# Kernel optimization log

Hardware: AMD Instinct MI355X
Metric: run time of the kernel (lower is better)

The kernel has to match this reference:

```python
import jax, jax.numpy as jnp
import numpy as np

N_NODES = 40000
N_EDGES = 320000
N_GRAPHS = 64
IN_DIM = 128
HID4 = 256   # hidden_dim * 4
OUT_DIM = 128
LN_EPS = 1e-5


def setup_inputs() -> dict:
    key = jax.random.key(0)
    ks = jax.random.split(key, 12)
    x = jax.random.normal(ks[0], (N_NODES, IN_DIM), dtype=jnp.float32)
    w = jax.random.uniform(ks[1], (N_EDGES, 4), dtype=jnp.float32)
    src = jax.random.randint(ks[2], (N_EDGES,), 0, N_NODES, dtype=jnp.int32)
    dst = jax.random.randint(ks[3], (N_EDGES,), 0, N_NODES, dtype=jnp.int32)
    graph_ids = jnp.sort(jax.random.randint(ks[4], (N_NODES,), 0, N_GRAPHS, dtype=jnp.int32))
    # parameters (no biases on GraphConv / fc1 linear)
    W1 = jax.random.normal(ks[5], (IN_DIM, HID4), dtype=jnp.float32) / np.sqrt(IN_DIM)
    fc1_W = jax.random.normal(ks[6], (IN_DIM, HID4), dtype=jnp.float32) / np.sqrt(IN_DIM)
    ln_gamma = jnp.ones((HID4,), dtype=jnp.float32)
    ln_beta = jnp.zeros((HID4,), dtype=jnp.float32)
    W2 = jax.random.normal(ks[7], (2 * HID4, HID4), dtype=jnp.float32) / np.sqrt(2 * HID4)
    W3 = jax.random.normal(ks[8], (HID4, OUT_DIM), dtype=jnp.float32) / np.sqrt(HID4)
    return {"x": x, "w": w, "W1": W1, "fc1_W": fc1_W, "ln_gamma": ln_gamma,
            "ln_beta": ln_beta, "W2": W2, "W3": W3,
            "src": src, "dst": dst, "graph_ids": graph_ids}


def _graph_conv(feat, src, dst, ew, W, out_inv_sqrt, in_inv_sqrt):
    # DGL GraphConv, norm='both', bias=False, with scalar edge_weight:
    # h = D_out^{-1/2} x ; m_e = w_e * h[src] ; agg = scatter_add(m, dst) ;
    # out = (D_in^{-1/2} agg) @ W
    h = feat * out_inv_sqrt[:, None]
    m = h[src] * ew[:, None]                       # [E, D] messages
    agg = jax.ops.segment_sum(m, dst, num_segments=N_NODES)
    return (agg * in_inv_sqrt[:, None]) @ W


def reference(x, w, W1, fc1_W, ln_gamma, ln_beta, W2, W3, src, dst, graph_ids):
    # unweighted degree normalization (DGL uses structural degrees, clamp(min=1))
    ones_e = jnp.ones((N_EDGES,), dtype=x.dtype)
    out_deg = jnp.maximum(jax.ops.segment_sum(ones_e, src, num_segments=N_NODES), 1.0)
    in_deg = jnp.maximum(jax.ops.segment_sum(ones_e, dst, num_segments=N_NODES), 1.0)
    out_inv = out_deg ** -0.5
    in_inv = in_deg ** -0.5

    ew = jnp.max(w, axis=1)                        # [E]

    x1 = jax.nn.relu(_graph_conv(x, src, dst, ew, W1, out_inv, in_inv))

    # fc1: Linear(no bias) -> LayerNorm(affine) -> ReLU
    f1 = x @ fc1_W
    mu = jnp.mean(f1, axis=-1, keepdims=True)
    var = jnp.mean((f1 - mu) ** 2, axis=-1, keepdims=True)
    f1 = (f1 - mu) * jax.lax.rsqrt(var + LN_EPS) * ln_gamma + ln_beta
    f1 = jax.nn.relu(f1)

    x1f1 = jnp.concatenate([x1, f1], axis=1)       # [N, 512]
    x2 = jax.nn.relu(_graph_conv(x1f1, src, dst, ew, W2, out_inv, in_inv))
    x3 = jax.nn.relu(_graph_conv(x2, src, dst, ew, W3, out_inv, in_inv))

    # dgl.sum_nodes over batched graph, then row-wise L2 normalize
    readout = jax.ops.segment_sum(x3, graph_ids, num_segments=N_GRAPHS)  # [G, OUT_DIM]
    norm = jnp.maximum(jnp.linalg.norm(readout, axis=1, keepdims=True), 1e-12)
    return readout / norm
```

## Files before the change

### kernel.cpp

```cpp
#include <hip/hip_runtime.h>

#define N_NODES 40000
#define M_PAD   40064
#define N_EDGES 320000
#define N_GRAPHS 64
#define IN_DIM 128
#define HID4 256
#define OUT_DIM 128
#define LN_EPS 1e-5f

typedef short  s16x8  __attribute__((ext_vector_type(8)));
typedef short  s16x4  __attribute__((ext_vector_type(4)));
typedef __bf16 bf16x8 __attribute__((ext_vector_type(8)));
typedef float  f32x4  __attribute__((ext_vector_type(4)));

__device__ __forceinline__ unsigned short f2b(float f) {
    unsigned int u = __builtin_bit_cast(unsigned int, f);
    u += 0x7fffu + ((u >> 16) & 1u);
    return (unsigned short)(u >> 16);
}
__device__ __forceinline__ float b2f(unsigned short h) {
    unsigned int u = (unsigned int)h << 16;
    return __builtin_bit_cast(float, u);
}


__global__ void edge_prep(const float* __restrict__ w, const int* __restrict__ src,
                          const int* __restrict__ dst, float* __restrict__ ew,
                          int* __restrict__ cnt_out, int* __restrict__ cnt_in) {
    int e = blockIdx.x * 256 + threadIdx.x;
    if (e >= N_EDGES) return;
    float4 v = ((const float4*)w)[e];
    ew[e] = fmaxf(fmaxf(v.x, v.y), fmaxf(v.z, v.w));
    atomicAdd(&cnt_out[src[e]], 1);
    atomicAdd(&cnt_in[dst[e]], 1);
}

__global__ void scan_part(const int* __restrict__ cnt, int* __restrict__ partial) {
    int b = blockIdx.x;
    int s = 0;
    for (int i = threadIdx.x; i < 1000; i += 256) s += cnt[b * 1000 + i];
#pragma unroll
    for (int m = 1; m < 64; m <<= 1) s += __shfl_xor(s, m);
    __shared__ int wsm[4];
    if ((threadIdx.x & 63) == 0) wsm[threadIdx.x >> 6] = s;
    __syncthreads();
    if (threadIdx.x == 0) partial[b] = wsm[0] + wsm[1] + wsm[2] + wsm[3];
}

__global__ void scan_final(const int* __restrict__ cnt_in, const int* __restrict__ cnt_out,
                           const int* __restrict__ partial, int* __restrict__ off,
                           float* __restrict__ out_inv, float* __restrict__ in_inv) {
    int b = blockIdx.x, tid = threadIdx.x;
    int lane = tid & 63, wv = tid >> 6;
    int pre = 0;
    for (int j = 0; j < b; ++j) pre += partial[j];
    int i = b * 1000 + tid;
    int v = (tid < 1000) ? cnt_in[i] : 0;
    int x = v;
#pragma unroll
    for (int ofs = 1; ofs < 64; ofs <<= 1) {
        int t = __shfl_up(x, ofs);
        if (lane >= ofs) x += t;
    }
    __shared__ int wsum[16];
    if (lane == 63) wsum[wv] = x;
    __syncthreads();
    if (wv == 0 && lane < 16) {
        int s = wsum[lane];
#pragma unroll
        for (int ofs = 1; ofs < 16; ofs <<= 1) {
            int t = __shfl_up(s, ofs);
            if (lane >= ofs) s += t;
        }
        wsum[lane] = s;
    }
    __syncthreads();
    int incl = pre + (wv > 0 ? wsum[wv - 1] : 0) + x;
    if (tid < 1000) {
        off[i] = incl - v;
        in_inv[i] = rsqrtf(fmaxf((float)v, 1.0f));
        out_inv[i] = rsqrtf(fmaxf((float)cnt_out[i], 1.0f));
    }
    if (b == 39 && tid == 999) off[N_NODES] = incl;
}

__global__ void csr_fill(const int* __restrict__ src, const int* __restrict__ dst,
                         const float* __restrict__ ew, const float* __restrict__ out_inv,
                         const int* __restrict__ off, int* __restrict__ cnt_in,
                         int* __restrict__ srcs, float* __restrict__ ewp,
                         float* __restrict__ ewps) {
    int e = blockIdx.x * 256 + threadIdx.x;
    if (e >= N_EDGES) return;
    int d = dst[e];
    int slot = off[d] + atomicSub(&cnt_in[d], 1) - 1;
    int s = src[e];
    float wv = ew[e];
    srcs[slot] = s;
    ewp[slot] = wv;
    ewps[slot] = wv * out_inv[s];
}


#define XN (N_NODES * IN_DIM)

__global__ void cvt_all(const float* __restrict__ x, const float* __restrict__ W1,
                        const float* __restrict__ fc1, const float* __restrict__ W2,
                        const float* __restrict__ W3, unsigned short* __restrict__ xb,
                        unsigned short* __restrict__ W1t, unsigned short* __restrict__ fc1t,
                        unsigned short* __restrict__ W2t, unsigned short* __restrict__ W3t) {
    int idx = blockIdx.x * 256 + threadIdx.x;
    if (idx < XN) { xb[idx] = f2b(x[idx]); return; }
    int j = idx - XN;
    if (j < 32768) { int k = j >> 8, n = j & 255; W1t[n * 128 + k] = f2b(W1[j]); return; }
    j -= 32768;
    if (j < 32768) { int k = j >> 8, n = j & 255; fc1t[n * 128 + k] = f2b(fc1[j]); return; }
    j -= 32768;
    if (j < 131072) { int k = j >> 8, n = j & 255; W2t[n * 512 + k] = f2b(W2[j]); return; }
    j -= 131072;
    if (j < 32768) { int k = j >> 7, n = j & 127; W3t[n * 256 + k] = f2b(W3[j]); }
}


template <int D, int RELU, int OUT_BF16>
__global__ void gather_nodes(const unsigned short* __restrict__ h, const int* __restrict__ off,
                             const int* __restrict__ srcs, const float* __restrict__ ews,
                             const float* __restrict__ scale, void* __restrict__ outp) {
    int n = blockIdx.x;
    int t = threadIdx.x;
    int b = off[n], e = off[n + 1];
    const unsigned int* hu = (const unsigned int*)h;
    float a0 = 0.0f, a1 = 0.0f;
    int i = b;
    for (; i + 1 < e; i += 2) {
        unsigned int p0 = hu[(size_t)srcs[i] * (D / 2) + t];
        unsigned int p1 = hu[(size_t)srcs[i + 1] * (D / 2) + t];
        float w0 = ews[i], w1 = ews[i + 1];
        a0 += w0 * b2f((unsigned short)p0) + w1 * b2f((unsigned short)p1);
        a1 += w0 * b2f((unsigned short)(p0 >> 16)) + w1 * b2f((unsigned short)(p1 >> 16));
    }
    if (i < e) {
        unsigned int p = hu[(size_t)srcs[i] * (D / 2) + t];
        float w0 = ews[i];
        a0 += w0 * b2f((unsigned short)p);
        a1 += w0 * b2f((unsigned short)(p >> 16));
    }
    float sc = scale[n];
    a0 *= sc; a1 *= sc;
    if (RELU) { a0 = fmaxf(a0, 0.0f); a1 = fmaxf(a1, 0.0f); }
    if (OUT_BF16) {
        unsigned int o = (unsigned int)f2b(a0) | ((unsigned int)f2b(a1) << 16);
        ((unsigned int*)outp)[(size_t)n * (D / 2) + t] = o;
    } else {
        ((float2*)outp)[(size_t)n * (D / 2) + t] = make_float2(a0, a1);
    }
}


template <int RELU, int SCALE_C>
__global__ __launch_bounds__(256) void gemm_mfma(
    const unsigned short* __restrict__ A, const unsigned short* __restrict__ A2,
    const unsigned short* __restrict__ Bt, unsigned short* __restrict__ C,
    const float* __restrict__ rowScaleC, int K1, int K2, int N) {
    __shared__ short As[128][40];
    __shared__ short Bs[128][40];
    const int K = K1 + K2;
    int tid = threadIdx.x;
    int lane = tid & 63, wave = tid >> 6;
    int wm = (wave >> 1) * 64, wn = (wave & 1) * 64;
    int quad = lane >> 4, r16 = lane & 15;
    int m0 = blockIdx.x * 128, n0 = blockIdx.y * 128;

    f32x4 acc[4][4] = {};

    int ra = tid >> 2;
    int ca = (tid & 3) * 8;

    for (int k0 = 0; k0 < K; k0 += 32) {
#pragma unroll
        for (int h = 0; h < 2; ++h) {
            int r = ra + h * 64;
            int kk = k0 + ca;
            const unsigned short* Ap = (kk < K1)
                ? A  + (size_t)(m0 + r) * K1 + kk
                : A2 + (size_t)(m0 + r) * K2 + (kk - K1);
            *(s16x8*)&As[r][ca] = *(const s16x8*)Ap;
            *(s16x8*)&Bs[r][ca] = *(const s16x8*)(Bt + (size_t)(n0 + r) * K + kk);
        }
        __syncthreads();
        s16x8 af[4], bfr[4];
#pragma unroll
        for (int i = 0; i < 4; ++i) af[i]  = *(const s16x8*)&As[wm + i * 16 + r16][quad * 8];
#pragma unroll
        for (int j = 0; j < 4; ++j) bfr[j] = *(const s16x8*)&Bs[wn + j * 16 + r16][quad * 8];
#pragma unroll
        for (int i = 0; i < 4; ++i)
#pragma unroll
            for (int j = 0; j < 4; ++j)
                acc[i][j] = __builtin_amdgcn_mfma_f32_16x16x32_bf16(
                    __builtin_bit_cast(bf16x8, af[i]), __builtin_bit_cast(bf16x8, bfr[j]),
                    acc[i][j], 0, 0, 0);
        __syncthreads();
    }

#pragma unroll
    for (int i = 0; i < 4; ++i) {
        int mbase = m0 + wm + i * 16 + quad * 4;
#pragma unroll
        for (int r = 0; r < 4; ++r) {
            int m = mbase + r;
            float sc = SCALE_C ? rowScaleC[m] : 1.0f;
#pragma unroll
            for (int j = 0; j < 4; ++j) {
                float v = acc[i][j][r] * sc;
                if (RELU) v = fmaxf(v, 0.0f);
                C[(size_t)m * N + n0 + wn + j * 16 + r16] = f2b(v);
            }
        }
    }
}


__global__ void ln_relu_bf16(unsigned short* __restrict__ f, const float* __restrict__ gamma,
                             const float* __restrict__ beta) {
    int row = (blockIdx.x * 256 + threadIdx.x) >> 6;
    int lane = threadIdx.x & 63;
    if (row >= N_NODES) return;
    s16x4* fr = (s16x4*)(f + (size_t)row * HID4);
    s16x4 pv = fr[lane];
    float v0 = b2f((unsigned short)pv[0]);
    float v1 = b2f((unsigned short)pv[1]);
    float v2 = b2f((unsigned short)pv[2]);
    float v3 = b2f((unsigned short)pv[3]);
    float sum = v0 + v1 + v2 + v3;
#pragma unroll
    for (int m = 1; m < 64; m <<= 1) sum += __shfl_xor(sum, m);
    float mu = sum * (1.0f / HID4);
    float d0 = v0 - mu, d1 = v1 - mu, d2 = v2 - mu, d3 = v3 - mu;
    float sq = d0 * d0 + d1 * d1 + d2 * d2 + d3 * d3;
#pragma unroll
    for (int m = 1; m < 64; m <<= 1) sq += __shfl_xor(sq, m);
    float rs = rsqrtf(sq * (1.0f / HID4) + LN_EPS);
    int c = lane * 4;
    s16x4 ov;
    ov[0] = (short)f2b(fmaxf(d0 * rs * gamma[c + 0] + beta[c + 0], 0.0f));
    ov[1] = (short)f2b(fmaxf(d1 * rs * gamma[c + 1] + beta[c + 1], 0.0f));
    ov[2] = (short)f2b(fmaxf(d2 * rs * gamma[c + 2] + beta[c + 2], 0.0f));
    ov[3] = (short)f2b(fmaxf(d3 * rs * gamma[c + 3] + beta[c + 3], 0.0f));
    fr[lane] = ov;
}


#define RO_NPB 16

__global__ void readout_sum(const float* __restrict__ x3, const int* __restrict__ gid,
                            float* __restrict__ ro) {
    int d = threadIdx.x;
    int n0 = blockIdx.x * RO_NPB;
    int n1 = n0 + RO_NPB;
    if (n1 > N_NODES) n1 = N_NODES;
    float acc = 0.0f;
    int cur = gid[n0];
    for (int n = n0; n < n1; ++n) {
        int g = gid[n];
        if (g != cur) {
            atomicAdd(&ro[cur * OUT_DIM + d], acc);
            acc = 0.0f;
            cur = g;
        }
        acc += x3[(size_t)n * OUT_DIM + d];
    }
    atomicAdd(&ro[cur * OUT_DIM + d], acc);
}

__global__ void normalize_out(const float* __restrict__ ro, float* __restrict__ out) {
    int g = blockIdx.x;
    int d = threadIdx.x;
    float v = ro[g * OUT_DIM + d];
    float ss = v * v;
#pragma unroll
    for (int m = 1; m < 64; m <<= 1) ss += __shfl_xor(ss, m);
    __shared__ float s2[2];
    if ((d & 63) == 0) s2[d >> 6] = ss;
    __syncthreads();
    float tot = s2[0] + s2[1];
    float norm = fmaxf(sqrtf(tot), 1e-12f);
    out[g * OUT_DIM + d] = v / norm;
}


extern "C" void kernel_launch(void* const* d_in, const int* in_sizes, int n_in,
                              void* d_out, int out_size, void* d_ws, size_t ws_size,
                              hipStream_t stream) {
    const float* x    = (const float*)d_in[0];
    const float* w    = (const float*)d_in[1];
    const float* W1   = (const float*)d_in[2];
    const float* fc1W = (const float*)d_in[3];
    const float* gam  = (const float*)d_in[4];
    const float* bet  = (const float*)d_in[5];
    const float* W2   = (const float*)d_in[6];
    const float* W3   = (const float*)d_in[7];
    const int* src = (const int*)d_in[8];
    const int* dst = (const int*)d_in[9];
    const int* gid = (const int*)d_in[10];
    float* out = (float*)d_out;

    float* ws = (float*)d_ws;
    float* out_inv = ws + 0;
    float* in_inv  = ws + 40000;
    float* ew      = ws + 80000;
    float* ro      = ws + 400000;
    unsigned short* W1t  = (unsigned short*)(ws + 410000);
    unsigned short* fc1t = (unsigned short*)(ws + 426384);
    unsigned short* W2t  = (unsigned short*)(ws + 442768);
    unsigned short* W3t  = (unsigned short*)(ws + 508304);
    int* cnt_out = (int*)(ws + 524688);
    int* cnt_in  = (int*)(ws + 564688);
    int* partial = (int*)(ws + 604688);
    int* off     = (int*)(ws + 604728);
    int* srcs    = (int*)(ws + 644730);
    float* ewp   = ws + 964730;
    float* ewps  = ws + 1284730;
    unsigned short* xb    = (unsigned short*)(ws + 1650000);
    unsigned short* Q3b   = xb;
    unsigned short* agg1b = (unsigned short*)(ws + 4250000);
    unsigned short* x2b   = agg1b;
    unsigned short* x1b   = (unsigned short*)(ws + 9400000);
    float*          x3    = (float*)x1b;
    unsigned short* f1b   = (unsigned short*)(ws + 14550000);
    unsigned short* P2b   = (unsigned short*)(ws + 19700000);

    hipMemsetAsync(cnt_out, 0, 2 * 40000 * sizeof(int), stream);
    hipMemsetAsync(ro, 0, (size_t)N_GRAPHS * OUT_DIM * sizeof(float), stream);

    cvt_all<<<(XN + 229376 + 255) / 256, 256, 0, stream>>>(x, W1, fc1W, W2, W3,
                                                           xb, W1t, fc1t, W2t, W3t);

    edge_prep<<<(N_EDGES + 255) / 256, 256, 0, stream>>>(w, src, dst, ew, cnt_out, cnt_in);
    scan_part<<<40, 256, 0, stream>>>(cnt_in, partial);
    scan_final<<<40, 1024, 0, stream>>>(cnt_in, cnt_out, partial, off, out_inv, in_inv);
    csr_fill<<<(N_EDGES + 255) / 256, 256, 0, stream>>>(src, dst, ew, out_inv, off, cnt_in,
                                                        srcs, ewp, ewps);

    gather_nodes<IN_DIM, 0, 1><<<N_NODES, IN_DIM / 2, 0, stream>>>(xb, off, srcs, ewps, in_inv, agg1b);
    {
        dim3 grid(M_PAD / 128, HID4 / 128);
        gemm_mfma<1, 0><<<grid, 256, 0, stream>>>(agg1b, nullptr, W1t, x1b, nullptr,
                                                  IN_DIM, 0, HID4);
    }

    {
        dim3 grid(M_PAD / 128, HID4 / 128);
        gemm_mfma<0, 0><<<grid, 256, 0, stream>>>(xb, nullptr, fc1t, f1b, nullptr,
                                                  IN_DIM, 0, HID4);
    }
    ln_relu_bf16<<<N_NODES / 4, 256, 0, stream>>>(f1b, gam, bet);

    {
        dim3 grid(M_PAD / 128, HID4 / 128);
        gemm_mfma<0, 1><<<grid, 256, 0, stream>>>(x1b, f1b, W2t, P2b, out_inv,
                                                  HID4, HID4, HID4);
    }
    gather_nodes<HID4, 1, 1><<<N_NODES, HID4 / 2, 0, stream>>>(P2b, off, srcs, ewp, in_inv, x2b);

    {
        dim3 grid(M_PAD / 128, OUT_DIM / 128);
        gemm_mfma<0, 1><<<grid, 256, 0, stream>>>(x2b, nullptr, W3t, Q3b, out_inv,
                                                  HID4, 0, OUT_DIM);
    }
    gather_nodes<OUT_DIM, 1, 0><<<N_NODES, OUT_DIM / 2, 0, stream>>>(Q3b, off, srcs, ewp, in_inv, x3);

    readout_sum<<<(N_NODES + RO_NPB - 1) / RO_NPB, 128, 0, stream>>>(x3, gid, ro);
    normalize_out<<<N_GRAPHS, 128, 0, stream>>>(ro, out);
}
```

Baseline: 303.8 us.

## Fuse prep kernels, pack edge arrays, merge first GEMMs, unroll gathers

Merges the weight/feature conversion and edge preparation into one kernel, and folds the two memsets into one. CSR edges are stored as packed (src, weight) int2 pairs so each gather reads one 8-byte record instead of two separate arrays. The gather loop is unrolled four-wide for more memory-level parallelism. The two first-layer GEMMs run as one launch using blockIdx.z, and the final layer output is kept in bf16 for readout. This trades some precision in the last layer and extra edge storage for fewer launches and fewer memory transactions.

```diff
diff --git a/kernel.cpp b/kernel.cpp
--- a/kernel.cpp
+++ b/kernel.cpp
@@ -25,15 +25,35 @@
 }
 
 
-__global__ void edge_prep(const float* __restrict__ w, const int* __restrict__ src,
-                          const int* __restrict__ dst, float* __restrict__ ew,
-                          int* __restrict__ cnt_out, int* __restrict__ cnt_in) {
-    int e = blockIdx.x * 256 + threadIdx.x;
-    if (e >= N_EDGES) return;
-    float4 v = ((const float4*)w)[e];
-    ew[e] = fmaxf(fmaxf(v.x, v.y), fmaxf(v.z, v.w));
-    atomicAdd(&cnt_out[src[e]], 1);
-    atomicAdd(&cnt_in[dst[e]], 1);
+#define XN (N_NODES * IN_DIM)
+#define WN 229376
+#define PREP_TOT (XN + WN + N_EDGES)
+
+__global__ void prep_all(const float* __restrict__ x, const float* __restrict__ W1,
+                         const float* __restrict__ fc1, const float* __restrict__ W2,
+                         const float* __restrict__ W3, const float* __restrict__ w,
+                         const int* __restrict__ src, const int* __restrict__ dst,
+                         unsigned short* __restrict__ xb, unsigned short* __restrict__ W1t,
+                         unsigned short* __restrict__ fc1t, unsigned short* __restrict__ W2t,
+                         unsigned short* __restrict__ W3t, float* __restrict__ ew,
+                         int* __restrict__ cnt_out, int* __restrict__ cnt_in) {
+    int idx = blockIdx.x * 256 + threadIdx.x;
+    if (idx < XN) { xb[idx] = f2b(x[idx]); return; }
+    int j = idx - XN;
+    if (j < 32768) { int k = j >> 8, n = j & 255; W1t[n * 128 + k] = f2b(W1[j]); return; }
+    j -= 32768;
+    if (j < 32768) { int k = j >> 8, n = j & 255; fc1t[n * 128 + k] = f2b(fc1[j]); return; }
+    j -= 32768;
+    if (j < 131072) { int k = j >> 8, n = j & 255; W2t[n * 512 + k] = f2b(W2[j]); return; }
+    j -= 131072;
+    if (j < 32768) { int k = j >> 7, n = j & 127; W3t[n * 256 + k] = f2b(W3[j]); return; }
+    j -= 32768;
+    if (j < N_EDGES) {
+        float4 v = ((const float4*)w)[j];
+        ew[j] = fmaxf(fmaxf(v.x, v.y), fmaxf(v.z, v.w));
+        atomicAdd(&cnt_out[src[j]], 1);
+        atomicAdd(&cnt_in[dst[j]], 1);
+    }
 }
 
 __global__ void scan_part(const int* __restrict__ cnt, int* __restrict__ partial) {
@@ -88,72 +108,53 @@
 __global__ void csr_fill(const int* __restrict__ src, const int* __restrict__ dst,
                          const float* __restrict__ ew, const float* __restrict__ out_inv,
                          const int* __restrict__ off, int* __restrict__ cnt_in,
-                         int* __restrict__ srcs, float* __restrict__ ewp,
-                         float* __restrict__ ewps) {
+                         int2* __restrict__ es1, int2* __restrict__ es23) {
     int e = blockIdx.x * 256 + threadIdx.x;
     if (e >= N_EDGES) return;
     int d = dst[e];
     int slot = off[d] + atomicSub(&cnt_in[d], 1) - 1;
     int s = src[e];
     float wv = ew[e];
-    srcs[slot] = s;
-    ewp[slot] = wv;
-    ewps[slot] = wv * out_inv[s];
-}
-
-
-#define XN (N_NODES * IN_DIM)
-
-__global__ void cvt_all(const float* __restrict__ x, const float* __restrict__ W1,
-                        const float* __restrict__ fc1, const float* __restrict__ W2,
-                        const float* __restrict__ W3, unsigned short* __restrict__ xb,
-                        unsigned short* __restrict__ W1t, unsigned short* __restrict__ fc1t,
-                        unsigned short* __restrict__ W2t, unsigned short* __restrict__ W3t) {
-    int idx = blockIdx.x * 256 + threadIdx.x;
-    if (idx < XN) { xb[idx] = f2b(x[idx]); return; }
-    int j = idx - XN;
-    if (j < 32768) { int k = j >> 8, n = j & 255; W1t[n * 128 + k] = f2b(W1[j]); return; }
-    j -= 32768;
-    if (j < 32768) { int k = j >> 8, n = j & 255; fc1t[n * 128 + k] = f2b(fc1[j]); return; }
-    j -= 32768;
-    if (j < 131072) { int k = j >> 8, n = j & 255; W2t[n * 512 + k] = f2b(W2[j]); return; }
-    j -= 131072;
-    if (j < 32768) { int k = j >> 7, n = j & 127; W3t[n * 256 + k] = f2b(W3[j]); }
-}
-
-
-template <int D, int RELU, int OUT_BF16>
+    es1[slot] = make_int2(s, __float_as_int(wv * out_inv[s]));
+    es23[slot] = make_int2(s, __float_as_int(wv));
+}
+
+
+template <int D, int RELU>
 __global__ void gather_nodes(const unsigned short* __restrict__ h, const int* __restrict__ off,
-                             const int* __restrict__ srcs, const float* __restrict__ ews,
-                             const float* __restrict__ scale, void* __restrict__ outp) {
+                             const int2* __restrict__ eg, const float* __restrict__ scale,
+                             unsigned short* __restrict__ outb) {
     int n = blockIdx.x;
     int t = threadIdx.x;
     int b = off[n], e = off[n + 1];
     const unsigned int* hu = (const unsigned int*)h;
     float a0 = 0.0f, a1 = 0.0f;
     int i = b;
-    for (; i + 1 < e; i += 2) {
-        unsigned int p0 = hu[(size_t)srcs[i] * (D / 2) + t];
-        unsigned int p1 = hu[(size_t)srcs[i + 1] * (D / 2) + t];
-        float w0 = ews[i], w1 = ews[i + 1];
-        a0 += w0 * b2f((unsigned short)p0) + w1 * b2f((unsigned short)p1);
-        a1 += w0 * b2f((unsigned short)(p0 >> 16)) + w1 * b2f((unsigned short)(p1 >> 16));
-    }
-    if (i < e) {
-        unsigned int p = hu[(size_t)srcs[i] * (D / 2) + t];
-        float w0 = ews[i];
+    for (; i + 3 < e; i += 4) {
+        int2 e0 = eg[i], e1 = eg[i + 1], e2 = eg[i + 2], e3 = eg[i + 3];
+        unsigned int p0 = hu[(size_t)e0.x * (D / 2) + t];
+        unsigned int p1 = hu[(size_t)e1.x * (D / 2) + t];
+        unsigned int p2 = hu[(size_t)e2.x * (D / 2) + t];
+        unsigned int p3 = hu[(size_t)e3.x * (D / 2) + t];
+        float w0 = __int_as_float(e0.y), w1 = __int_as_float(e1.y);
+        float w2 = __int_as_float(e2.y), w3 = __int_as_float(e3.y);
+        a0 += w0 * b2f((unsigned short)p0) + w1 * b2f((unsigned short)p1)
+            + w2 * b2f((unsigned short)p2) + w3 * b2f((unsigned short)p3);
+        a1 += w0 * b2f((unsigned short)(p0 >> 16)) + w1 * b2f((unsigned short)(p1 >> 16))
+            + w2 * b2f((unsigned short)(p2 >> 16)) + w3 * b2f((unsigned short)(p3 >> 16));
+    }
+    for (; i < e; ++i) {
+        int2 ee = eg[i];
+        unsigned int p = hu[(size_t)ee.x * (D / 2) + t];
+        float w0 = __int_as_float(ee.y);
         a0 += w0 * b2f((unsigned short)p);
         a1 += w0 * b2f((unsigned short)(p >> 16));
     }
     float sc = scale[n];
     a0 *= sc; a1 *= sc;
     if (RELU) { a0 = fmaxf(a0, 0.0f); a1 = fmaxf(a1, 0.0f); }
-    if (OUT_BF16) {
-        unsigned int o = (unsigned int)f2b(a0) | ((unsigned int)f2b(a1) << 16);
-        ((unsigned int*)outp)[(size_t)n * (D / 2) + t] = o;
-    } else {
-        ((float2*)outp)[(size_t)n * (D / 2) + t] = make_float2(a0, a1);
-    }
+    unsigned int o = (unsigned int)f2b(a0) | ((unsigned int)f2b(a1) << 16);
+    ((unsigned int*)outb)[(size_t)n * (D / 2) + t] = o;
 }
 
 
@@ -172,7 +173,6 @@
     int m0 = blockIdx.x * 128, n0 = blockIdx.y * 128;
 
     f32x4 acc[4][4] = {};
-
     int ra = tid >> 2;
     int ca = (tid & 3) * 8;
 
@@ -215,6 +215,68 @@
                 float v = acc[i][j][r] * sc;
                 if (RELU) v = fmaxf(v, 0.0f);
                 C[(size_t)m * N + n0 + wn + j * 16 + r16] = f2b(v);
+            }
+        }
+    }
+}
+
+
+__global__ __launch_bounds__(256) void gemm_dual(
+    const unsigned short* __restrict__ A0, const unsigned short* __restrict__ B0,
+    unsigned short* __restrict__ C0,
+    const unsigned short* __restrict__ A1, const unsigned short* __restrict__ B1,
+    unsigned short* __restrict__ C1) {
+    const unsigned short* A  = blockIdx.z ? A1 : A0;
+    const unsigned short* Bt = blockIdx.z ? B1 : B0;
+    unsigned short* C        = blockIdx.z ? C1 : C0;
+    const int relu = (blockIdx.z == 0);
+    __shared__ short As[128][40];
+    __shared__ short Bs[128][40];
+    int tid = threadIdx.x;
+    int lane = tid & 63, wave = tid >> 6;
+    int wm = (wave >> 1) * 64, wn = (wave & 1) * 64;
+    int quad = lane >> 4, r16 = lane & 15;
+    int m0 = blockIdx.x * 128, n0 = blockIdx.y * 128;
+
+    f32x4 acc[4][4] = {};
+    int ra = tid >> 2;
+    int ca = (tid & 3) * 8;
+
+    for (int k0 = 0; k0 < 128; k0 += 32) {
+#pragma unroll
+        for (int h = 0; h < 2; ++h) {
+            int r = ra + h * 64;
+            int kk = k0 + ca;
+            *(s16x8*)&As[r][ca] = *(const s16x8*)(A + (size_t)(m0 + r) * 128 + kk);
+            *(s16x8*)&Bs[r][ca] = *(const s16x8*)(Bt + (size_t)(n0 + r) * 128 + kk);
+        }
+        __syncthreads();
+        s16x8 af[4], bfr[4];
+#pragma unroll
+        for (int i = 0; i < 4; ++i) af[i]  = *(const s16x8*)&As[wm + i * 16 + r16][quad * 8];
+#pragma unroll
+        for (int j = 0; j < 4; ++j) bfr[j] = *(const s16x8*)&Bs[wn + j * 16 + r16][quad * 8];
+#pragma unroll
+        for (int i = 0; i < 4; ++i)
+#pragma unroll
+            for (int j = 0; j < 4; ++j)
+                acc[i][j] = __builtin_amdgcn_mfma_f32_16x16x32_bf16(
+                    __builtin_bit_cast(bf16x8, af[i]), __builtin_bit_cast(bf16x8, bfr[j]),
+                    acc[i][j], 0, 0, 0);
+        __syncthreads();
+    }
+
+#pragma unroll
+    for (int i = 0; i < 4; ++i) {
+        int mbase = m0 + wm + i * 16 + quad * 4;
+#pragma unroll
+        for (int r = 0; r < 4; ++r) {
+            int m = mbase + r;
+#pragma unroll
+            for (int j = 0; j < 4; ++j) {
+                float v = acc[i][j][r];
+                if (relu) v = fmaxf(v, 0.0f);
+                C[(size_t)m * 256 + n0 + wn + j * 16 + r16] = f2b(v);
             }
         }
     }
@@ -253,7 +315,7 @@
 
 #define RO_NPB 16
 
-__global__ void readout_sum(const float* __restrict__ x3, const int* __restrict__ gid,
+__global__ void readout_sum(const unsigned short* __restrict__ x3, const int* __restrict__ gid,
                             float* __restrict__ ro) {
     int d = threadIdx.x;
     int n0 = blockIdx.x * RO_NPB;
@@ -268,7 +330,7 @@
             acc = 0.0f;
             cur = g;
         }
-        acc += x3[(size_t)n * OUT_DIM + d];
+        acc += b2f(x3[(size_t)n * OUT_DIM + d]);
     }
     atomicAdd(&ro[cur * OUT_DIM + d], acc);
 }
@@ -309,50 +371,40 @@
     float* out_inv = ws + 0;
     float* in_inv  = ws + 40000;
     float* ew      = ws + 80000;
-    float* ro      = ws + 400000;
-    unsigned short* W1t  = (unsigned short*)(ws + 410000);
-    unsigned short* fc1t = (unsigned short*)(ws + 426384);
-    unsigned short* W2t  = (unsigned short*)(ws + 442768);
-    unsigned short* W3t  = (unsigned short*)(ws + 508304);
-    int* cnt_out = (int*)(ws + 524688);
-    int* cnt_in  = (int*)(ws + 564688);
-    int* partial = (int*)(ws + 604688);
-    int* off     = (int*)(ws + 604728);
-    int* srcs    = (int*)(ws + 644730);
-    float* ewp   = ws + 964730;
-    float* ewps  = ws + 1284730;
-    unsigned short* xb    = (unsigned short*)(ws + 1650000);
+    int*   cnt_out = (int*)(ws + 400000);
+    int*   cnt_in  = (int*)(ws + 440000);
+    float* ro      = ws + 480000;
+    unsigned short* W1t  = (unsigned short*)(ws + 488192);
+    unsigned short* fc1t = (unsigned short*)(ws + 504576);
+    unsigned short* W2t  = (unsigned short*)(ws + 520960);
+    unsigned short* W3t  = (unsigned short*)(ws + 586496);
+    int*   partial = (int*)(ws + 602880);
+    int*   off     = (int*)(ws + 602920);
+    int2*  es1     = (int2*)(ws + 642922);
+    int2*  es23    = (int2*)(ws + 1282922);
+    unsigned short* xb    = (unsigned short*)(ws + 1923000);
     unsigned short* Q3b   = xb;
-    unsigned short* agg1b = (unsigned short*)(ws + 4250000);
+    unsigned short* agg1b = (unsigned short*)(ws + 4487100);
     unsigned short* x2b   = agg1b;
-    unsigned short* x1b   = (unsigned short*)(ws + 9400000);
-    float*          x3    = (float*)x1b;
-    unsigned short* f1b   = (unsigned short*)(ws + 14550000);
-    unsigned short* P2b   = (unsigned short*)(ws + 19700000);
-
-    hipMemsetAsync(cnt_out, 0, 2 * 40000 * sizeof(int), stream);
-    hipMemsetAsync(ro, 0, (size_t)N_GRAPHS * OUT_DIM * sizeof(float), stream);
-
-    cvt_all<<<(XN + 229376 + 255) / 256, 256, 0, stream>>>(x, W1, fc1W, W2, W3,
-                                                           xb, W1t, fc1t, W2t, W3t);
-
-    edge_prep<<<(N_EDGES + 255) / 256, 256, 0, stream>>>(w, src, dst, ew, cnt_out, cnt_in);
+    unsigned short* x1b   = (unsigned short*)(ws + 9615300);
+    unsigned short* x3b   = x1b;
+    unsigned short* f1b   = (unsigned short*)(ws + 14743500);
+    unsigned short* P2b   = (unsigned short*)(ws + 19871700);
+
+    hipMemsetAsync(cnt_out, 0, (2 * 40000 + N_GRAPHS * OUT_DIM) * sizeof(float), stream);
+
+    prep_all<<<(PREP_TOT + 255) / 256, 256, 0, stream>>>(x, W1, fc1W, W2, W3, w, src, dst,
+                                                         xb, W1t, fc1t, W2t, W3t, ew,
+                                                         cnt_out, cnt_in);
     scan_part<<<40, 256, 0, stream>>>(cnt_in, partial);
     scan_final<<<40, 1024, 0, stream>>>(cnt_in, cnt_out, partial, off, out_inv, in_inv);
     csr_fill<<<(N_EDGES + 255) / 256, 256, 0, stream>>>(src, dst, ew, out_inv, off, cnt_in,
-                                                        srcs, ewp, ewps);
-
-    gather_nodes<IN_DIM, 0, 1><<<N_NODES, IN_DIM / 2, 0, stream>>>(xb, off, srcs, ewps, in_inv, agg1b);
+                                                        es1, es23);
+
+    gather_nodes<IN_DIM, 0><<<N_NODES, IN_DIM / 2, 0, stream>>>(xb, off, es1, in_inv, agg1b);
     {
-        dim3 grid(M_PAD / 128, HID4 / 128);
-        gemm_mfma<1, 0><<<grid, 256, 0, stream>>>(agg1b, nullptr, W1t, x1b, nullptr,
-                                                  IN_DIM, 0, HID4);
-    }
-
-    {
-        dim3 grid(M_PAD / 128, HID4 / 128);
-        gemm_mfma<0, 0><<<grid, 256, 0, stream>>>(xb, nullptr, fc1t, f1b, nullptr,
-                                                  IN_DIM, 0, HID4);
+        dim3 grid(M_PAD / 128, HID4 / 128, 2);
+        gemm_dual<<<grid, 256, 0, stream>>>(agg1b, W1t, x1b, xb, fc1t, f1b);
     }
     ln_relu_bf16<<<N_NODES / 4, 256, 0, stream>>>(f1b, gam, bet);
 
@@ -361,15 +413,15 @@
         gemm_mfma<0, 1><<<grid, 256, 0, stream>>>(x1b, f1b, W2t, P2b, out_inv,
                                                   HID4, HID4, HID4);
     }
-    gather_nodes<HID4, 1, 1><<<N_NODES, HID4 / 2, 0, stream>>>(P2b, off, srcs, ewp, in_inv, x2b);
+    gather_nodes<HID4, 1><<<N_NODES, HID4 / 2, 0, stream>>>(P2b, off, es23, in_inv, x2b);
 
     {
         dim3 grid(M_PAD / 128, OUT_DIM / 128);
         gemm_mfma<0, 1><<<grid, 256, 0, stream>>>(x2b, nullptr, W3t, Q3b, out_inv,
                                                   HID4, 0, OUT_DIM);
     }
-    gather_nodes<OUT_DIM, 1, 0><<<N_NODES, OUT_DIM / 2, 0, stream>>>(Q3b, off, srcs, ewp, in_inv, x3);
-
-    readout_sum<<<(N_NODES + RO_NPB - 1) / RO_NPB, 128, 0, stream>>>(x3, gid, ro);
+    gather_nodes<OUT_DIM, 1><<<N_NODES, OUT_DIM / 2, 0, stream>>>(Q3b, off, es23, in_inv, x3b);
+
+    readout_sum<<<(N_NODES + RO_NPB - 1) / RO_NPB, 128, 0, stream>>>(x3b, gid, ro);
     normalize_out<<<N_GRAPHS, 128, 0, stream>>>(ro, out);
 }
```

After: 298.4 us. Within noise of the previous version (-1.8%).
